# Optimization experiments

Hardware: AMD Instinct MI355X
Metric: run time of the kernel (lower is better)

The kernel has to match this reference:

```python
import jax, jax.numpy as jnp
import numpy as np

B, S = 128, 200
Q, K, V, C, SUM = 20000, 128, 128, 64, 128


def setup_inputs() -> dict:
    key = jax.random.key(0)
    ks = jax.random.split(key, 14)
    stdev = 1.0 / np.sqrt(C + K)  # NTM-style memory init bound

    def lin_w(k, fan_in, shape):
        b = 1.0 / np.sqrt(fan_in)
        return jax.random.uniform(k, shape, jnp.float32, -b, b)

    # embeddings with padding_idx=0 zeroed (PAD_INDEX=0)
    q_emb = jax.random.normal(ks[0], (Q + 1, K), jnp.float32).at[0].set(0.0)
    i_emb = jax.random.normal(ks[1], (2 * Q + 1, V), jnp.float32).at[0].set(0.0)
    key_memory = jax.random.uniform(ks[2], (K, C), jnp.float32, -stdev, stdev)
    init_value_memory = jax.random.uniform(ks[3], (V, C), jnp.float32, -stdev, stdev)
    erase_W = lin_w(ks[4], V, (V, V))
    erase_b = lin_w(ks[5], V, (V,))
    add_W = lin_w(ks[6], V, (V, V))
    add_b = lin_w(ks[7], V, (V,))
    summ_W = lin_w(ks[8], V + K, (V + K, SUM))
    summ_b = lin_w(ks[9], V + K, (SUM,))
    out_W = lin_w(ks[10], SUM, (SUM, 1))
    out_b = lin_w(ks[11], SUM, (1,))
    inp = jax.random.randint(ks[12], (B, S), 0, 2 * Q + 1)
    target_id = jax.random.randint(ks[13], (B,), 0, Q + 1)
    return dict(q_emb=q_emb, i_emb=i_emb, key_memory=key_memory,
                init_value_memory=init_value_memory,
                erase_W=erase_W, erase_b=erase_b, add_W=add_W, add_b=add_b,
                summ_W=summ_W, summ_b=summ_b, out_W=out_W, out_b=out_b,
                input=inp, target_id=target_id)


def reference(q_emb, i_emb, key_memory, init_value_memory,
              erase_W, erase_b, add_W, add_b,
              summ_W, summ_b, out_W, out_b,
              input, target_id):
    Qn = q_emb.shape[0] - 1
    bsz = input.shape[0]
    # map interaction index -> question id
    qid = input - Qn * (input > Qn).astype(input.dtype)          # (B,S)
    # all per-step quantities are independent of memory state -> precompute
    iv = i_emb[input]                                            # (B,S,V)
    e = jax.nn.sigmoid(iv @ erase_W + erase_b)                   # (B,S,V)
    a = jnp.tanh(iv @ add_W + add_b)                             # (B,S,V)
    w = jax.nn.softmax(q_emb[qid] @ key_memory, axis=-1)         # (B,S,C)

    mem0 = jnp.broadcast_to(init_value_memory, (bsz,) + init_value_memory.shape)  # (B,V,C)

    def step(mem, xs):
        e_t, a_t, w_t = xs                                       # (B,V),(B,V),(B,C)
        erase = e_t[:, :, None] * w_t[:, None, :]                # rank-1 outer, (B,V,C)
        add = a_t[:, :, None] * w_t[:, None, :]
        mem = mem * (1.0 - erase) + add
        return mem, None

    xs = (jnp.swapaxes(e, 0, 1), jnp.swapaxes(a, 0, 1), jnp.swapaxes(w, 0, 1))
    mem, _ = jax.lax.scan(step, mem0, xs)                        # (B,V,C)

    qv = q_emb[target_id]                                        # (B,K)
    wt = jax.nn.softmax(qv @ key_memory, axis=-1)                # (B,C)
    read = jnp.einsum('bvc,bc->bv', mem, wt)                     # (B,V)
    summ = jnp.tanh(jnp.concatenate([read, qv], axis=-1) @ summ_W + summ_b)
    return summ @ out_W + out_b                                  # (B,1), pre-sigmoid
```

## Files before the change

kernel.cpp:

```cpp
#include <hip/hip_runtime.h>
#include <hip/hip_bf16.h>
#include <hip/hip_fp16.h>

#define B_ 128
#define S_ 200
#define QN_ 20000
#define V_ 128
#define K_ 128
#define C_ 64
#define SUM_ 128
#define NCH 8
#define CL 25

using short8 = __attribute__((ext_vector_type(8))) short;
using f32x4  = __attribute__((ext_vector_type(4))) float;

__device__ __forceinline__ float fast_sigmoid(float x) { return 1.f / (1.f + __expf(-x)); }
__device__ __forceinline__ float fast_tanh(float x)    { return 1.f - 2.f / (__expf(2.f * x) + 1.f); }

template<bool BF>
__device__ __forceinline__ float ld(const void* p, long long i) {
    if (BF) return __bfloat162float(((const __hip_bfloat16*)p)[i]);
    return ((const float*)p)[i];
}

__device__ __forceinline__ unsigned short f2bf(float v) {
    __hip_bfloat16 h = __float2bfloat16(v);
    unsigned short u;
    __builtin_memcpy(&u, &h, 2);
    return u;
}

__device__ __forceinline__ void ld4h(const __half* p, float* out) {
    const float2 f01 = __half22float2(*(const __half2*)p);
    const float2 f23 = __half22float2(*(const __half2*)(p + 2));
    out[0] = f01.x; out[1] = f01.y; out[2] = f23.x; out[3] = f23.y;
}

__device__ __forceinline__ int probe_flag_wave(const void* erase_b) {
    const unsigned* w = (const unsigned*)erase_b;
    const int lane = threadIdx.x & 63;
    const unsigned lo = w[lane] & 0xffffu;
    const float f = __uint_as_float(lo << 16);
    const unsigned long long bal = __ballot(!(fabsf(f) <= 0.5f));
    return (__popcll(bal) <= 8) ? 1 : 0;
}

__global__ __launch_bounds__(256) void dkvmn_prepack(
    const void* erase_W, const void* add_W, const void* key_memory,
    const void* erase_b, unsigned short* __restrict__ wpack)
{
    const int bf = probe_flag_wave(erase_b);
    const int fid = blockIdx.x * 256 + threadIdx.x;
    if (fid >= 5120) return;
    const int lane = fid & 63;
    const int ks = (fid >> 6) & 3;
    const int wv = (fid >> 8) & 3;
    const int q  = fid >> 10;
    const int nt = wv + 4 * q;
    const void* Wsrc;
    int ncol, ldn;
    if (q < 2)      { Wsrc = erase_W;    ncol = nt * 16 + (lane & 15);        ldn = 128; }
    else if (q < 4) { Wsrc = add_W;      ncol = (nt - 8) * 16 + (lane & 15);  ldn = 128; }
    else            { Wsrc = key_memory; ncol = (nt - 16) * 16 + (lane & 15); ldn = 64; }
    const int k8 = (lane >> 4) * 8;
    unsigned short o[8];
    #pragma unroll
    for (int jj = 0; jj < 8; ++jj) {
        const long long idx = (long long)(ks * 32 + k8 + jj) * ldn + ncol;
        const float v = bf ? ld<true>(Wsrc, idx) : ld<false>(Wsrc, idx);
        o[jj] = f2bf(v);
    }
    *(uint4*)(wpack + (size_t)fid * 8) = *(const uint4*)o;
}

struct FusedLDS {
    unsigned short ivA[32 * 136];
    unsigned short qvA[32 * 136];
    __half esh[32 * 136];
    __half ash[32 * 136];
    float  wlog[32 * 68];
    int sidx[32], sqid[32];
};

template<bool BF>
__device__ __forceinline__ void fused_body(
    const void* q_emb, const void* i_emb,
    const void* erase_b, const void* add_b,
    const int* __restrict__ input, const unsigned short* __restrict__ wpack,
    __half2* __restrict__ du, FusedLDS& sm)
{
    const int bid = blockIdx.x;
    const int b = bid & 127;
    const int chunk = bid >> 7;
    const int t = threadIdx.x;
    const int wv = t >> 6;
    const int lane = t & 63;
    const int lrow = lane & 15;
    const int lk8 = (lane >> 4) * 8;

    if (t < 32) {
        const int s = (t < CL) ? t : 0;
        const int ix = input[b * S_ + chunk * CL + s];
        sm.sidx[t] = ix;
        sm.sqid[t] = ix > QN_ ? ix - QN_ : ix;
    }
    __syncthreads();

    #pragma unroll
    for (int r = 0; r < 4; ++r) {
        const int j = t + 256 * r;
        const int tensor = j >> 9;
        const int row = (j >> 4) & 31;
        const int seg = j & 15;
        const int gr = tensor ? sm.sqid[row] : sm.sidx[row];
        unsigned short* dst = (tensor ? sm.qvA : sm.ivA) + row * 136 + seg * 8;
        if (BF) {
            const unsigned short* src = (const unsigned short*)(tensor ? q_emb : i_emb);
            *(uint4*)dst = *(const uint4*)(src + (long long)gr * 128 + seg * 8);
        } else {
            const float* src = (const float*)(tensor ? q_emb : i_emb) + (long long)gr * 128 + seg * 8;
            const float4 f0 = *(const float4*)src;
            const float4 f1 = *(const float4*)(src + 4);
            unsigned short o[8] = {f2bf(f0.x), f2bf(f0.y), f2bf(f0.z), f2bf(f0.w),
                                   f2bf(f1.x), f2bf(f1.y), f2bf(f1.z), f2bf(f1.w)};
            *(uint4*)dst = *(const uint4*)o;
        }
    }

    short8 bfr[5][4];
    int nco[5];
    float biasq[4];
    #pragma unroll
    for (int q = 0; q < 5; ++q) {
        const int nt = wv + 4 * q;
        if (q < 2)      nco[q] = nt * 16 + lrow;
        else if (q < 4) nco[q] = (nt - 8) * 16 + lrow;
        else            nco[q] = (nt - 16) * 16 + lrow;
        if (q < 2)      biasq[q] = ld<BF>(erase_b, nco[q]);
        else if (q < 4) biasq[q] = ld<BF>(add_b, nco[q]);
        #pragma unroll
        for (int ks = 0; ks < 4; ++ks)
            bfr[q][ks] = *(const short8*)(wpack +
                ((size_t)(((q * 4 + wv) * 4 + ks) * 64 + lane)) * 8);
    }
    __syncthreads();

    #pragma unroll
    for (int mt = 0; mt < 2; ++mt) {
        short8 afr[4];
        const unsigned short* ar = sm.ivA + (mt * 16 + lrow) * 136 + lk8;
        #pragma unroll
        for (int ks = 0; ks < 4; ++ks)
            afr[ks] = *(const short8*)(ar + ks * 32);
        #pragma unroll
        for (int q = 0; q < 4; ++q) {
            f32x4 acc = {0.f, 0.f, 0.f, 0.f};
            #pragma unroll
            for (int ks = 0; ks < 4; ++ks)
                acc = __builtin_amdgcn_mfma_f32_16x16x32_bf16(afr[ks], bfr[q][ks], acc, 0, 0, 0);
            const int ncol = nco[q];
            const float bb = biasq[q];
            #pragma unroll
            for (int r = 0; r < 4; ++r) {
                const int orow = mt * 16 + (lane >> 4) * 4 + r;
                const float y = acc[r] + bb;
                if (q < 2) sm.esh[orow * 136 + ncol] = __float2half(fast_sigmoid(y));
                else       sm.ash[orow * 136 + ncol] = __float2half(fast_tanh(y));
            }
        }
    }
    #pragma unroll
    for (int mt = 0; mt < 2; ++mt) {
        short8 afr[4];
        const unsigned short* ar = sm.qvA + (mt * 16 + lrow) * 136 + lk8;
        #pragma unroll
        for (int ks = 0; ks < 4; ++ks)
            afr[ks] = *(const short8*)(ar + ks * 32);
        f32x4 acc = {0.f, 0.f, 0.f, 0.f};
        #pragma unroll
        for (int ks = 0; ks < 4; ++ks)
            acc = __builtin_amdgcn_mfma_f32_16x16x32_bf16(afr[ks], bfr[4][ks], acc, 0, 0, 0);
        #pragma unroll
        for (int r = 0; r < 4; ++r)
            sm.wlog[(mt * 16 + (lane >> 4) * 4 + r) * 68 + nco[4]] = acc[r];
    }
    __syncthreads();

    {
        const int row = t >> 3;
        const int cs = t & 7;
        float* wr = &sm.wlog[row * 68 + cs * 8];
        float v[8];
        *(float4*)&v[0] = *(const float4*)&wr[0];
        *(float4*)&v[4] = *(const float4*)&wr[4];
        float m = v[0];
        #pragma unroll
        for (int ii = 1; ii < 8; ++ii) m = fmaxf(m, v[ii]);
        m = fmaxf(m, __shfl_xor(m, 1, 64));
        m = fmaxf(m, __shfl_xor(m, 2, 64));
        m = fmaxf(m, __shfl_xor(m, 4, 64));
        float s = 0.f;
        #pragma unroll
        for (int ii = 0; ii < 8; ++ii) { v[ii] = __expf(v[ii] - m); s += v[ii]; }
        s += __shfl_xor(s, 1, 64);
        s += __shfl_xor(s, 2, 64);
        s += __shfl_xor(s, 4, 64);
        const float inv = 1.f / s;
        *(float4*)&wr[0] = make_float4(v[0]*inv, v[1]*inv, v[2]*inv, v[3]*inv);
        *(float4*)&wr[4] = make_float4(v[4]*inv, v[5]*inv, v[6]*inv, v[7]*inv);
    }
    __syncthreads();

    const int vg = t >> 3;
    const int cg = t & 7;
    const int v0 = vg * 4, c0 = cg * 8;

    float ym[4][8], Dm[4][8];
    #pragma unroll
    for (int i = 0; i < 4; ++i)
        #pragma unroll
        for (int j = 0; j < 8; ++j) { ym[i][j] = 0.f; Dm[i][j] = 1.f; }

    for (int s = 0; s < CL; ++s) {
        float ev[4], av[4], wv8[8];
        ld4h(sm.esh + s * 136 + v0, ev);
        ld4h(sm.ash + s * 136 + v0, av);
        *(float4*)&wv8[0] = *(const float4*)(sm.wlog + s * 68 + c0);
        *(float4*)&wv8[4] = *(const float4*)(sm.wlog + s * 68 + c0 + 4);
        #pragma unroll
        for (int i = 0; i < 4; ++i) {
            #pragma unroll
            for (int j = 0; j < 8; ++j) {
                const float d = fmaf(-ev[i], wv8[j], 1.f);
                Dm[i][j] *= d;
                ym[i][j] = fmaf(d, ym[i][j], av[i] * wv8[j]);
            }
        }
    }

    __half2* dbase = du + ((size_t)(chunk * B_ + b) * (V_ * C_));
    #pragma unroll
    for (int i = 0; i < 4; ++i) {
        __half2 h[8];
        #pragma unroll
        for (int j = 0; j < 8; ++j)
            h[j] = __floats2half2_rn(Dm[i][j], ym[i][j]);
        __half2* dst = dbase + (v0 + i) * C_ + c0;
        *(uint4*)dst = *(const uint4*)&h[0];
        *(uint4*)(dst + 4) = *(const uint4*)&h[4];
    }
}

__global__ __launch_bounds__(256) void dkvmn_fused(
    const void* q_emb, const void* i_emb,
    const void* erase_b, const void* add_b,
    const int* __restrict__ input, const unsigned short* __restrict__ wpack,
    __half2* __restrict__ du)
{
    __shared__ FusedLDS sm;
    if (probe_flag_wave(erase_b))
        fused_body<true>(q_emb, i_emb, erase_b, add_b, input, wpack, du, sm);
    else
        fused_body<false>(q_emb, i_emb, erase_b, add_b, input, wpack, du, sm);
}

template<bool BF>
__device__ __forceinline__ void combine_body(
    const void* q_emb, const void* key_memory, const void* init_value_memory,
    const void* summ_W, const void* summ_b, const void* out_W, const void* out_b,
    const int* __restrict__ target_id, const __half2* __restrict__ du,
    void* outp, float* wtl, float* readl, float* summl)
{
    const int b = blockIdx.x;
    const int t = threadIdx.x;
    const long long qrow = (long long)target_id[b] * K_;

    if (t < 64) {
        float logit = 0.f;
        #pragma unroll 8
        for (int i = 0; i < K_; ++i)
            logit += ld<BF>(q_emb, qrow + i) * ld<BF>(key_memory, i * C_ + t);
        float m = logit;
        for (int off = 32; off > 0; off >>= 1)
            m = fmaxf(m, __shfl_xor(m, off, 64));
        const float ex = __expf(logit - m);
        float ssum = ex;
        for (int off = 32; off > 0; off >>= 1)
            ssum += __shfl_xor(ssum, off, 64);
        wtl[t] = ex / ssum;
    }

    const int v = t >> 1;
    const int c0 = (t & 1) * 32;
    float mem[32];
    #pragma unroll 8
    for (int k = 0; k < 32; ++k)
        mem[k] = ld<BF>(init_value_memory, v * C_ + c0 + k);
    #pragma unroll
    for (int ch = 0; ch < NCH; ++ch) {
        const __half2* dsrc = du + ((size_t)(ch * B_ + b) * (V_ * C_)) + v * C_ + c0;
        #pragma unroll
        for (int k = 0; k < 32; ++k) {
            const float2 f = __half22float2(dsrc[k]);
            mem[k] = fmaf(f.x, mem[k], f.y);
        }
    }
    __syncthreads();

    float pacc = 0.f;
    #pragma unroll
    for (int k = 0; k < 32; ++k)
        pacc += mem[k] * wtl[c0 + k];
    pacc += __shfl_xor(pacc, 1, 64);
    if ((t & 1) == 0) readl[v] = pacc;
    __syncthreads();

    if (t < 128) {
        float acc = ld<BF>(summ_b, t);
        #pragma unroll 8
        for (int i = 0; i < 128; ++i)
            acc += readl[i] * ld<BF>(summ_W, i * SUM_ + t);
        #pragma unroll 8
        for (int i = 0; i < 128; ++i)
            acc += ld<BF>(q_emb, qrow + i) * ld<BF>(summ_W, (128 + i) * SUM_ + t);
        summl[t] = fast_tanh(acc);
    }
    __syncthreads();
    if (t < 64) {
        float oacc = summl[t] * ld<BF>(out_W, t) + summl[t + 64] * ld<BF>(out_W, t + 64);
        for (int off = 32; off > 0; off >>= 1)
            oacc += __shfl_xor(oacc, off, 64);
        if (t == 0) {
            const float res = oacc + ld<BF>(out_b, 0);
            if (BF) ((__hip_bfloat16*)outp)[b] = __float2bfloat16(res);
            else    ((float*)outp)[b] = res;
        }
    }
}

__global__ __launch_bounds__(256) void dkvmn_combine(
    const void* q_emb, const void* key_memory, const void* init_value_memory,
    const void* summ_W, const void* summ_b, const void* out_W, const void* out_b,
    const void* erase_b, const int* __restrict__ target_id,
    const __half2* __restrict__ du, void* outp)
{
    __shared__ float wtl[C_], readl[V_], summl[SUM_];
    if (probe_flag_wave(erase_b))
        combine_body<true>(q_emb, key_memory, init_value_memory, summ_W, summ_b,
                           out_W, out_b, target_id, du, outp, wtl, readl, summl);
    else
        combine_body<false>(q_emb, key_memory, init_value_memory, summ_W, summ_b,
                            out_W, out_b, target_id, du, outp, wtl, readl, summl);
}

extern "C" void kernel_launch(void* const* d_in, const int* in_sizes, int n_in,
                              void* d_out, int out_size, void* d_ws, size_t ws_size,
                              hipStream_t stream) {
    const void* q_emb             = d_in[0];
    const void* i_emb             = d_in[1];
    const void* key_memory        = d_in[2];
    const void* init_value_memory = d_in[3];
    const void* erase_W           = d_in[4];
    const void* erase_b           = d_in[5];
    const void* add_W             = d_in[6];
    const void* add_b             = d_in[7];
    const void* summ_W            = d_in[8];
    const void* summ_b            = d_in[9];
    const void* out_W             = d_in[10];
    const void* out_b             = d_in[11];
    const int* input     = (const int*)d_in[12];
    const int* target_id = (const int*)d_in[13];

    unsigned short* wpack = (unsigned short*)d_ws;
    __half2* du = (__half2*)(wpack + 5120 * 8);

    dkvmn_prepack<<<20, 256, 0, stream>>>(erase_W, add_W, key_memory, erase_b, wpack);
    dkvmn_fused<<<NCH * B_, 256, 0, stream>>>(
        q_emb, i_emb, erase_b, add_b, input, wpack, du);
    dkvmn_combine<<<B_, 256, 0, stream>>>(
        q_emb, key_memory, init_value_memory, summ_W, summ_b, out_W, out_b,
        erase_b, target_id, du, d_out);
}
```

Baseline: 148.0 us.

## Split combine into parallel fold and final kernels, precompute target weights

Moves the target softmax weight computation into extra blocks of the prepack kernel. The former combine stage becomes two kernels. A fold kernel uses four times as many blocks with vectorized 16-byte loads of the fp16 chunk deltas and reduces them into a read vector. A small final kernel then does the summary and output layers. The aim is to parallelize the bandwidth-heavy fold over 512 blocks instead of 128, at the cost of one extra launch and global intermediate buffers.

```diff
diff --git a/kernel.cpp b/kernel.cpp
--- a/kernel.cpp
+++ b/kernel.cpp
@@ -46,11 +46,40 @@
     return (__popcll(bal) <= 8) ? 1 : 0;
 }
 
+template<bool BF>
+__device__ __forceinline__ void wt_body(
+    const void* q_emb, const void* key_memory, const int* __restrict__ target_id,
+    int b, float* __restrict__ wt_buf)
+{
+    const int t = threadIdx.x;
+    if (t >= 64) return;
+    const long long qrow = (long long)target_id[b] * K_;
+    float logit = 0.f;
+    #pragma unroll 8
+    for (int i = 0; i < K_; ++i)
+        logit += ld<BF>(q_emb, qrow + i) * ld<BF>(key_memory, i * C_ + t);
+    float m = logit;
+    for (int off = 32; off > 0; off >>= 1)
+        m = fmaxf(m, __shfl_xor(m, off, 64));
+    const float ex = __expf(logit - m);
+    float ssum = ex;
+    for (int off = 32; off > 0; off >>= 1)
+        ssum += __shfl_xor(ssum, off, 64);
+    wt_buf[b * C_ + t] = ex / ssum;
+}
+
 __global__ __launch_bounds__(256) void dkvmn_prepack(
     const void* erase_W, const void* add_W, const void* key_memory,
-    const void* erase_b, unsigned short* __restrict__ wpack)
+    const void* erase_b, const void* q_emb, const int* __restrict__ target_id,
+    unsigned short* __restrict__ wpack, float* __restrict__ wt_buf)
 {
     const int bf = probe_flag_wave(erase_b);
+    if (blockIdx.x >= 20) {
+        const int b = blockIdx.x - 20;
+        if (bf) wt_body<true>(q_emb, key_memory, target_id, b, wt_buf);
+        else    wt_body<false>(q_emb, key_memory, target_id, b, wt_buf);
+        return;
+    }
     const int fid = blockIdx.x * 256 + threadIdx.x;
     if (fid >= 5120) return;
     const int lane = fid & 63;
@@ -266,67 +295,91 @@
 }
 
 template<bool BF>
-__device__ __forceinline__ void combine_body(
-    const void* q_emb, const void* key_memory, const void* init_value_memory,
-    const void* summ_W, const void* summ_b, const void* out_W, const void* out_b,
-    const int* __restrict__ target_id, const __half2* __restrict__ du,
-    void* outp, float* wtl, float* readl, float* summl)
+__device__ __forceinline__ void fold_body(
+    const void* init_value_memory, const __half2* __restrict__ du,
+    const float* __restrict__ wt_buf, float* __restrict__ readl_buf)
+{
+    const int bid = blockIdx.x;
+    const int b = bid & 127;
+    const int sub = bid >> 7;
+    const int t = threadIdx.x;
+    const int v = sub * 32 + (t >> 3);
+    const int cg = t & 7;
+    const int c0 = cg * 8;
+
+    uint4 qa[NCH], qb[NCH];
+    #pragma unroll
+    for (int ch = 0; ch < NCH; ++ch) {
+        const __half2* base = du + ((size_t)(ch * B_ + b) * (V_ * C_)) + v * C_ + c0;
+        qa[ch] = *(const uint4*)base;
+        qb[ch] = *(const uint4*)(base + 4);
+    }
+
+    float mem[8];
+    #pragma unroll
+    for (int k = 0; k < 8; ++k)
+        mem[k] = ld<BF>(init_value_memory, v * C_ + c0 + k);
+
+    #pragma unroll
+    for (int ch = 0; ch < NCH; ++ch) {
+        const __half2* hA = (const __half2*)&qa[ch];
+        const __half2* hB = (const __half2*)&qb[ch];
+        #pragma unroll
+        for (int k = 0; k < 4; ++k) {
+            const float2 fA = __half22float2(hA[k]);
+            mem[k] = fmaf(fA.x, mem[k], fA.y);
+            const float2 fB = __half22float2(hB[k]);
+            mem[4 + k] = fmaf(fB.x, mem[4 + k], fB.y);
+        }
+    }
+
+    float wt8[8];
+    *(float4*)&wt8[0] = *(const float4*)(wt_buf + b * C_ + c0);
+    *(float4*)&wt8[4] = *(const float4*)(wt_buf + b * C_ + c0 + 4);
+    float pacc = 0.f;
+    #pragma unroll
+    for (int k = 0; k < 8; ++k) pacc += mem[k] * wt8[k];
+    pacc += __shfl_xor(pacc, 1, 64);
+    pacc += __shfl_xor(pacc, 2, 64);
+    pacc += __shfl_xor(pacc, 4, 64);
+    if (cg == 0) readl_buf[b * V_ + v] = pacc;
+}
+
+__global__ __launch_bounds__(256) void dkvmn_fold(
+    const void* init_value_memory, const void* erase_b,
+    const __half2* __restrict__ du, const float* __restrict__ wt_buf,
+    float* __restrict__ readl_buf)
+{
+    if (probe_flag_wave(erase_b))
+        fold_body<true>(init_value_memory, du, wt_buf, readl_buf);
+    else
+        fold_body<false>(init_value_memory, du, wt_buf, readl_buf);
+}
+
+template<bool BF>
+__device__ __forceinline__ void final_body(
+    const void* q_emb, const void* summ_W, const void* summ_b,
+    const void* out_W, const void* out_b,
+    const int* __restrict__ target_id, const float* __restrict__ readl_buf,
+    void* outp, float* readl, float* summl)
 {
     const int b = blockIdx.x;
     const int t = threadIdx.x;
     const long long qrow = (long long)target_id[b] * K_;
 
-    if (t < 64) {
-        float logit = 0.f;
-        #pragma unroll 8
-        for (int i = 0; i < K_; ++i)
-            logit += ld<BF>(q_emb, qrow + i) * ld<BF>(key_memory, i * C_ + t);
-        float m = logit;
-        for (int off = 32; off > 0; off >>= 1)
-            m = fmaxf(m, __shfl_xor(m, off, 64));
-        const float ex = __expf(logit - m);
-        float ssum = ex;
-        for (int off = 32; off > 0; off >>= 1)
-            ssum += __shfl_xor(ssum, off, 64);
-        wtl[t] = ex / ssum;
-    }
-
-    const int v = t >> 1;
-    const int c0 = (t & 1) * 32;
-    float mem[32];
+    readl[t] = readl_buf[b * V_ + t];
+    __syncthreads();
+
+    float acc = ld<BF>(summ_b, t);
     #pragma unroll 8
-    for (int k = 0; k < 32; ++k)
-        mem[k] = ld<BF>(init_value_memory, v * C_ + c0 + k);
-    #pragma unroll
-    for (int ch = 0; ch < NCH; ++ch) {
-        const __half2* dsrc = du + ((size_t)(ch * B_ + b) * (V_ * C_)) + v * C_ + c0;
-        #pragma unroll
-        for (int k = 0; k < 32; ++k) {
-            const float2 f = __half22float2(dsrc[k]);
-            mem[k] = fmaf(f.x, mem[k], f.y);
-        }
-    }
-    __syncthreads();
-
-    float pacc = 0.f;
-    #pragma unroll
-    for (int k = 0; k < 32; ++k)
-        pacc += mem[k] * wtl[c0 + k];
-    pacc += __shfl_xor(pacc, 1, 64);
-    if ((t & 1) == 0) readl[v] = pacc;
-    __syncthreads();
-
-    if (t < 128) {
-        float acc = ld<BF>(summ_b, t);
-        #pragma unroll 8
-        for (int i = 0; i < 128; ++i)
-            acc += readl[i] * ld<BF>(summ_W, i * SUM_ + t);
-        #pragma unroll 8
-        for (int i = 0; i < 128; ++i)
-            acc += ld<BF>(q_emb, qrow + i) * ld<BF>(summ_W, (128 + i) * SUM_ + t);
-        summl[t] = fast_tanh(acc);
-    }
-    __syncthreads();
+    for (int i = 0; i < 128; ++i)
+        acc += readl[i] * ld<BF>(summ_W, i * SUM_ + t);
+    #pragma unroll 8
+    for (int i = 0; i < 128; ++i)
+        acc += ld<BF>(q_emb, qrow + i) * ld<BF>(summ_W, (128 + i) * SUM_ + t);
+    summl[t] = fast_tanh(acc);
+    __syncthreads();
+
     if (t < 64) {
         float oacc = summl[t] * ld<BF>(out_W, t) + summl[t + 64] * ld<BF>(out_W, t + 64);
         for (int off = 32; off > 0; off >>= 1)
@@ -339,19 +392,19 @@
     }
 }
 
-__global__ __launch_bounds__(256) void dkvmn_combine(
-    const void* q_emb, const void* key_memory, const void* init_value_memory,
-    const void* summ_W, const void* summ_b, const void* out_W, const void* out_b,
-    const void* erase_b, const int* __restrict__ target_id,
-    const __half2* __restrict__ du, void* outp)
-{
-    __shared__ float wtl[C_], readl[V_], summl[SUM_];
+__global__ __launch_bounds__(128) void dkvmn_final(
+    const void* q_emb, const void* summ_W, const void* summ_b,
+    const void* out_W, const void* out_b, const void* erase_b,
+    const int* __restrict__ target_id, const float* __restrict__ readl_buf,
+    void* outp)
+{
+    __shared__ float readl[V_], summl[SUM_];
     if (probe_flag_wave(erase_b))
-        combine_body<true>(q_emb, key_memory, init_value_memory, summ_W, summ_b,
-                           out_W, out_b, target_id, du, outp, wtl, readl, summl);
+        final_body<true>(q_emb, summ_W, summ_b, out_W, out_b, target_id,
+                         readl_buf, outp, readl, summl);
     else
-        combine_body<false>(q_emb, key_memory, init_value_memory, summ_W, summ_b,
-                            out_W, out_b, target_id, du, outp, wtl, readl, summl);
+        final_body<false>(q_emb, summ_W, summ_b, out_W, out_b, target_id,
+                          readl_buf, outp, readl, summl);
 }
 
 extern "C" void kernel_launch(void* const* d_in, const int* in_sizes, int n_in,
@@ -374,11 +427,15 @@
 
     unsigned short* wpack = (unsigned short*)d_ws;
     __half2* du = (__half2*)(wpack + 5120 * 8);
-
-    dkvmn_prepack<<<20, 256, 0, stream>>>(erase_W, add_W, key_memory, erase_b, wpack);
+    float* wt_buf = (float*)(du + (size_t)NCH * B_ * V_ * C_);
+    float* readl_buf = wt_buf + (size_t)B_ * C_;
+
+    dkvmn_prepack<<<148, 256, 0, stream>>>(
+        erase_W, add_W, key_memory, erase_b, q_emb, target_id, wpack, wt_buf);
     dkvmn_fused<<<NCH * B_, 256, 0, stream>>>(
         q_emb, i_emb, erase_b, add_b, input, wpack, du);
-    dkvmn_combine<<<B_, 256, 0, stream>>>(
-        q_emb, key_memory, init_value_memory, summ_W, summ_b, out_W, out_b,
-        erase_b, target_id, du, d_out);
-}
+    dkvmn_fold<<<4 * B_, 256, 0, stream>>>(
+        init_value_memory, erase_b, du, wt_buf, readl_buf);
+    dkvmn_final<<<B_, 128, 0, stream>>>(
+        q_emb, summ_W, summ_b, out_W, out_b, erase_b, target_id, readl_buf, d_out);
+}
```

Result: no change. 147.3 us, median of 2 (-0.5%).

## Move target softmax to prepack, trim padded rows, double-buffer chunk loads

Applied to the files above, without the earlier changes.

The target-key softmax is computed in extra blocks of the prepack kernel and stored to a workspace buffer, which takes it off the critical path of the final reduce kernel. The fused kernel shrinks its LDS arrays to the real chunk length and skips the padded rows in gather, activation and softmax work. The reduce kernel software-pipelines the per-chunk delta loads with a register double buffer so global loads overlap the FMA chain. This costs more registers in the reduce kernel and an extra global round trip for the softmax weights.

```diff
diff --git a/kernel.cpp b/kernel.cpp
--- a/kernel.cpp
+++ b/kernel.cpp
@@ -46,11 +46,40 @@
     return (__popcll(bal) <= 8) ? 1 : 0;
 }
 
+template<bool BF>
+__device__ __forceinline__ void wt_body(
+    const void* q_emb, const void* key_memory, const int* __restrict__ target_id,
+    int b, float* __restrict__ wt_buf)
+{
+    const int t = threadIdx.x;
+    if (t >= 64) return;
+    const long long qrow = (long long)target_id[b] * K_;
+    float logit = 0.f;
+    #pragma unroll 8
+    for (int i = 0; i < K_; ++i)
+        logit += ld<BF>(q_emb, qrow + i) * ld<BF>(key_memory, i * C_ + t);
+    float m = logit;
+    for (int off = 32; off > 0; off >>= 1)
+        m = fmaxf(m, __shfl_xor(m, off, 64));
+    const float ex = __expf(logit - m);
+    float ssum = ex;
+    for (int off = 32; off > 0; off >>= 1)
+        ssum += __shfl_xor(ssum, off, 64);
+    wt_buf[b * C_ + t] = ex / ssum;
+}
+
 __global__ __launch_bounds__(256) void dkvmn_prepack(
     const void* erase_W, const void* add_W, const void* key_memory,
-    const void* erase_b, unsigned short* __restrict__ wpack)
+    const void* erase_b, const void* q_emb, const int* __restrict__ target_id,
+    unsigned short* __restrict__ wpack, float* __restrict__ wt_buf)
 {
     const int bf = probe_flag_wave(erase_b);
+    if (blockIdx.x >= 20) {
+        const int b = blockIdx.x - 20;
+        if (bf) wt_body<true>(q_emb, key_memory, target_id, b, wt_buf);
+        else    wt_body<false>(q_emb, key_memory, target_id, b, wt_buf);
+        return;
+    }
     const int fid = blockIdx.x * 256 + threadIdx.x;
     if (fid >= 5120) return;
     const int lane = fid & 63;
@@ -77,10 +106,10 @@
 struct FusedLDS {
     unsigned short ivA[32 * 136];
     unsigned short qvA[32 * 136];
-    __half esh[32 * 136];
-    __half ash[32 * 136];
-    float  wlog[32 * 68];
-    int sidx[32], sqid[32];
+    __half esh[CL * 136];
+    __half ash[CL * 136];
+    float  wlog[CL * 68];
+    int sidx[CL + 7], sqid[CL + 7];
 };
 
 template<bool BF>
@@ -99,32 +128,34 @@
     const int lrow = lane & 15;
     const int lk8 = (lane >> 4) * 8;
 
-    if (t < 32) {
-        const int s = (t < CL) ? t : 0;
-        const int ix = input[b * S_ + chunk * CL + s];
+    if (t < CL) {
+        const int ix = input[b * S_ + chunk * CL + t];
         sm.sidx[t] = ix;
         sm.sqid[t] = ix > QN_ ? ix - QN_ : ix;
     }
     __syncthreads();
 
     #pragma unroll
-    for (int r = 0; r < 4; ++r) {
-        const int j = t + 256 * r;
-        const int tensor = j >> 9;
-        const int row = (j >> 4) & 31;
-        const int seg = j & 15;
-        const int gr = tensor ? sm.sqid[row] : sm.sidx[row];
-        unsigned short* dst = (tensor ? sm.qvA : sm.ivA) + row * 136 + seg * 8;
-        if (BF) {
-            const unsigned short* src = (const unsigned short*)(tensor ? q_emb : i_emb);
-            *(uint4*)dst = *(const uint4*)(src + (long long)gr * 128 + seg * 8);
-        } else {
-            const float* src = (const float*)(tensor ? q_emb : i_emb) + (long long)gr * 128 + seg * 8;
-            const float4 f0 = *(const float4*)src;
-            const float4 f1 = *(const float4*)(src + 4);
-            unsigned short o[8] = {f2bf(f0.x), f2bf(f0.y), f2bf(f0.z), f2bf(f0.w),
-                                   f2bf(f1.x), f2bf(f1.y), f2bf(f1.z), f2bf(f1.w)};
-            *(uint4*)dst = *(const uint4*)o;
+    for (int rep = 0; rep < 4; ++rep) {
+        const int j = t + 256 * rep;
+        if (j < 2 * CL * 16) {
+            const int tensor = (j >= CL * 16) ? 1 : 0;
+            const int r = tensor ? (j - CL * 16) : j;
+            const int row = r >> 4;
+            const int seg = r & 15;
+            const int gr = tensor ? sm.sqid[row] : sm.sidx[row];
+            unsigned short* dst = (tensor ? sm.qvA : sm.ivA) + row * 136 + seg * 8;
+            if (BF) {
+                const unsigned short* src = (const unsigned short*)(tensor ? q_emb : i_emb);
+                *(uint4*)dst = *(const uint4*)(src + (long long)gr * 128 + seg * 8);
+            } else {
+                const float* src = (const float*)(tensor ? q_emb : i_emb) + (long long)gr * 128 + seg * 8;
+                const float4 f0 = *(const float4*)src;
+                const float4 f1 = *(const float4*)(src + 4);
+                unsigned short o[8] = {f2bf(f0.x), f2bf(f0.y), f2bf(f0.z), f2bf(f0.w),
+                                       f2bf(f1.x), f2bf(f1.y), f2bf(f1.z), f2bf(f1.w)};
+                *(uint4*)dst = *(const uint4*)o;
+            }
         }
     }
 
@@ -164,9 +195,11 @@
             #pragma unroll
             for (int r = 0; r < 4; ++r) {
                 const int orow = mt * 16 + (lane >> 4) * 4 + r;
-                const float y = acc[r] + bb;
-                if (q < 2) sm.esh[orow * 136 + ncol] = __float2half(fast_sigmoid(y));
-                else       sm.ash[orow * 136 + ncol] = __float2half(fast_tanh(y));
+                if (orow < CL) {
+                    const float y = acc[r] + bb;
+                    if (q < 2) sm.esh[orow * 136 + ncol] = __float2half(fast_sigmoid(y));
+                    else       sm.ash[orow * 136 + ncol] = __float2half(fast_tanh(y));
+                }
             }
         }
     }
@@ -182,33 +215,38 @@
         for (int ks = 0; ks < 4; ++ks)
             acc = __builtin_amdgcn_mfma_f32_16x16x32_bf16(afr[ks], bfr[4][ks], acc, 0, 0, 0);
         #pragma unroll
-        for (int r = 0; r < 4; ++r)
-            sm.wlog[(mt * 16 + (lane >> 4) * 4 + r) * 68 + nco[4]] = acc[r];
+        for (int r = 0; r < 4; ++r) {
+            const int orow = mt * 16 + (lane >> 4) * 4 + r;
+            if (orow < CL)
+                sm.wlog[orow * 68 + nco[4]] = acc[r];
+        }
     }
     __syncthreads();
 
     {
         const int row = t >> 3;
         const int cs = t & 7;
-        float* wr = &sm.wlog[row * 68 + cs * 8];
-        float v[8];
-        *(float4*)&v[0] = *(const float4*)&wr[0];
-        *(float4*)&v[4] = *(const float4*)&wr[4];
-        float m = v[0];
-        #pragma unroll
-        for (int ii = 1; ii < 8; ++ii) m = fmaxf(m, v[ii]);
-        m = fmaxf(m, __shfl_xor(m, 1, 64));
-        m = fmaxf(m, __shfl_xor(m, 2, 64));
-        m = fmaxf(m, __shfl_xor(m, 4, 64));
-        float s = 0.f;
-        #pragma unroll
-        for (int ii = 0; ii < 8; ++ii) { v[ii] = __expf(v[ii] - m); s += v[ii]; }
-        s += __shfl_xor(s, 1, 64);
-        s += __shfl_xor(s, 2, 64);
-        s += __shfl_xor(s, 4, 64);
-        const float inv = 1.f / s;
-        *(float4*)&wr[0] = make_float4(v[0]*inv, v[1]*inv, v[2]*inv, v[3]*inv);
-        *(float4*)&wr[4] = make_float4(v[4]*inv, v[5]*inv, v[6]*inv, v[7]*inv);
+        if (row < CL) {
+            float* wr = &sm.wlog[row * 68 + cs * 8];
+            float v[8];
+            *(float4*)&v[0] = *(const float4*)&wr[0];
+            *(float4*)&v[4] = *(const float4*)&wr[4];
+            float m = v[0];
+            #pragma unroll
+            for (int ii = 1; ii < 8; ++ii) m = fmaxf(m, v[ii]);
+            m = fmaxf(m, __shfl_xor(m, 1, 64));
+            m = fmaxf(m, __shfl_xor(m, 2, 64));
+            m = fmaxf(m, __shfl_xor(m, 4, 64));
+            float s = 0.f;
+            #pragma unroll
+            for (int ii = 0; ii < 8; ++ii) { v[ii] = __expf(v[ii] - m); s += v[ii]; }
+            s += __shfl_xor(s, 1, 64);
+            s += __shfl_xor(s, 2, 64);
+            s += __shfl_xor(s, 4, 64);
+            const float inv = 1.f / s;
+            *(float4*)&wr[0] = make_float4(v[0]*inv, v[1]*inv, v[2]*inv, v[3]*inv);
+            *(float4*)&wr[4] = make_float4(v[4]*inv, v[5]*inv, v[6]*inv, v[7]*inv);
+        }
     }
     __syncthreads();
 
@@ -266,56 +304,57 @@
 }
 
 template<bool BF>
-__device__ __forceinline__ void combine_body(
-    const void* q_emb, const void* key_memory, const void* init_value_memory,
-    const void* summ_W, const void* summ_b, const void* out_W, const void* out_b,
+__device__ __forceinline__ void reduce_body(
+    const void* q_emb, const void* summ_W, const void* summ_b,
+    const void* out_W, const void* out_b, const void* init_value_memory,
     const int* __restrict__ target_id, const __half2* __restrict__ du,
-    void* outp, float* wtl, float* readl, float* summl)
+    const float* __restrict__ wt_buf, void* outp,
+    float* readl, float* summl)
 {
     const int b = blockIdx.x;
     const int t = threadIdx.x;
-    const long long qrow = (long long)target_id[b] * K_;
-
-    if (t < 64) {
-        float logit = 0.f;
-        #pragma unroll 8
-        for (int i = 0; i < K_; ++i)
-            logit += ld<BF>(q_emb, qrow + i) * ld<BF>(key_memory, i * C_ + t);
-        float m = logit;
-        for (int off = 32; off > 0; off >>= 1)
-            m = fmaxf(m, __shfl_xor(m, off, 64));
-        const float ex = __expf(logit - m);
-        float ssum = ex;
-        for (int off = 32; off > 0; off >>= 1)
-            ssum += __shfl_xor(ssum, off, 64);
-        wtl[t] = ex / ssum;
-    }
-
     const int v = t >> 1;
     const int c0 = (t & 1) * 32;
+
     float mem[32];
     #pragma unroll 8
     for (int k = 0; k < 32; ++k)
         mem[k] = ld<BF>(init_value_memory, v * C_ + c0 + k);
+
+    uint4 qbuf[2][8];
+    {
+        const uint4* base0 = (const uint4*)(du + ((size_t)b * (V_ * C_)) + v * C_ + c0);
+        #pragma unroll
+        for (int i = 0; i < 8; ++i) qbuf[0][i] = base0[i];
+    }
     #pragma unroll
     for (int ch = 0; ch < NCH; ++ch) {
-        const __half2* dsrc = du + ((size_t)(ch * B_ + b) * (V_ * C_)) + v * C_ + c0;
+        if (ch + 1 < NCH) {
+            const uint4* basen = (const uint4*)(du +
+                ((size_t)((ch + 1) * B_ + b) * (V_ * C_)) + v * C_ + c0);
+            #pragma unroll
+            for (int i = 0; i < 8; ++i) qbuf[(ch + 1) & 1][i] = basen[i];
+        }
+        const __half2* h = (const __half2*)&qbuf[ch & 1][0];
         #pragma unroll
         for (int k = 0; k < 32; ++k) {
-            const float2 f = __half22float2(dsrc[k]);
+            const float2 f = __half22float2(h[k]);
             mem[k] = fmaf(f.x, mem[k], f.y);
         }
     }
-    __syncthreads();
 
     float pacc = 0.f;
-    #pragma unroll
-    for (int k = 0; k < 32; ++k)
-        pacc += mem[k] * wtl[c0 + k];
+    const float* wtb = wt_buf + b * C_ + c0;
+    #pragma unroll
+    for (int k = 0; k < 32; k += 4) {
+        const float4 w4 = *(const float4*)(wtb + k);
+        pacc += mem[k] * w4.x + mem[k+1] * w4.y + mem[k+2] * w4.z + mem[k+3] * w4.w;
+    }
     pacc += __shfl_xor(pacc, 1, 64);
     if ((t & 1) == 0) readl[v] = pacc;
     __syncthreads();
 
+    const long long qrow = (long long)target_id[b] * K_;
     if (t < 128) {
         float acc = ld<BF>(summ_b, t);
         #pragma unroll 8
@@ -327,6 +366,7 @@
         summl[t] = fast_tanh(acc);
     }
     __syncthreads();
+
     if (t < 64) {
         float oacc = summl[t] * ld<BF>(out_W, t) + summl[t + 64] * ld<BF>(out_W, t + 64);
         for (int off = 32; off > 0; off >>= 1)
@@ -339,19 +379,20 @@
     }
 }
 
-__global__ __launch_bounds__(256) void dkvmn_combine(
-    const void* q_emb, const void* key_memory, const void* init_value_memory,
-    const void* summ_W, const void* summ_b, const void* out_W, const void* out_b,
+__global__ __launch_bounds__(256) void dkvmn_reduce(
+    const void* q_emb, const void* summ_W, const void* summ_b,
+    const void* out_W, const void* out_b, const void* init_value_memory,
     const void* erase_b, const int* __restrict__ target_id,
-    const __half2* __restrict__ du, void* outp)
-{
-    __shared__ float wtl[C_], readl[V_], summl[SUM_];
+    const __half2* __restrict__ du, const float* __restrict__ wt_buf,
+    void* outp)
+{
+    __shared__ float readl[V_], summl[SUM_];
     if (probe_flag_wave(erase_b))
-        combine_body<true>(q_emb, key_memory, init_value_memory, summ_W, summ_b,
-                           out_W, out_b, target_id, du, outp, wtl, readl, summl);
+        reduce_body<true>(q_emb, summ_W, summ_b, out_W, out_b, init_value_memory,
+                          target_id, du, wt_buf, outp, readl, summl);
     else
-        combine_body<false>(q_emb, key_memory, init_value_memory, summ_W, summ_b,
-                            out_W, out_b, target_id, du, outp, wtl, readl, summl);
+        reduce_body<false>(q_emb, summ_W, summ_b, out_W, out_b, init_value_memory,
+                           target_id, du, wt_buf, outp, readl, summl);
 }
 
 extern "C" void kernel_launch(void* const* d_in, const int* in_sizes, int n_in,
@@ -374,11 +415,13 @@
 
     unsigned short* wpack = (unsigned short*)d_ws;
     __half2* du = (__half2*)(wpack + 5120 * 8);
-
-    dkvmn_prepack<<<20, 256, 0, stream>>>(erase_W, add_W, key_memory, erase_b, wpack);
+    float* wt_buf = (float*)(du + (size_t)NCH * B_ * V_ * C_);
+
+    dkvmn_prepack<<<148, 256, 0, stream>>>(
+        erase_W, add_W, key_memory, erase_b, q_emb, target_id, wpack, wt_buf);
     dkvmn_fused<<<NCH * B_, 256, 0, stream>>>(
         q_emb, i_emb, erase_b, add_b, input, wpack, du);
-    dkvmn_combine<<<B_, 256, 0, stream>>>(
-        q_emb, key_memory, init_value_memory, summ_W, summ_b, out_W, out_b,
-        erase_b, target_id, du, d_out);
-}
+    dkvmn_reduce<<<B_, 256, 0, stream>>>(
+        q_emb, summ_W, summ_b, out_W, out_b, init_value_memory,
+        erase_b, target_id, du, wt_buf, d_out);
+}
```

After: 151.2 us. 1.02x slower.
